# Performance work log

Measured on AMD Instinct MI355X. Metric: run time of the kernel, lower is better.

## Reference

```python
import jax, jax.numpy as jnp
import numpy as np

N = 8192
FEAT = 128
HID = 128
EMB = 128
NHEADS = 2
RO_HID = 256
G_EMB = 128
ALPHA = 0.2          # LeakyReLU negative slope
NEG_INF = -9e15      # matches -9000000000000000.0 in the torch source


def _xavier(k, shape, gain=1.0):
    fan_in, fan_out = shape[-2], shape[-1]
    s = gain * np.sqrt(2.0 / (fan_in + fan_out))
    return jax.random.normal(k, shape, jnp.float32) * jnp.float32(s)


def setup_inputs() -> dict:
    key = jax.random.key(0)
    ks = jax.random.split(key, 10)
    adj = jax.random.randint(ks[0], (N, N), 0, 2, jnp.int32)          # dense 0/1 adjacency
    x = jax.random.normal(ks[1], (N, FEAT), jnp.float32)
    W_heads = _xavier(ks[2], (NHEADS, FEAT, HID), gain=1.414)
    a_heads = _xavier(ks[3], (NHEADS, 2 * HID, 1), gain=1.414)
    W_out = _xavier(ks[4], (NHEADS * HID, EMB), gain=1.414)
    a_out = _xavier(ks[5], (2 * EMB, 1), gain=1.414)
    ge_w1 = _xavier(ks[6], (FEAT + EMB, RO_HID))
    ge_b1 = jnp.zeros((RO_HID,), jnp.float32)
    ge_w2 = _xavier(ks[7], (RO_HID, G_EMB))
    ge_b2 = jnp.zeros((G_EMB,), jnp.float32)
    return dict(adj=adj, feature_matrix=x, W_heads=W_heads, a_heads=a_heads,
                W_out=W_out, a_out=a_out, ge_w1=ge_w1, ge_b1=ge_b1,
                ge_w2=ge_w2, ge_b2=ge_b2, supply=0)


def _gat_layer(x, mask, W, a, concat):
    # Faithful to GraphAttentionLayer: e_ij = leakyrelu([Wh_i || Wh_j] @ a).
    # The concat-then-matmul decomposes exactly as Wh@a[:F] + (Wh@a[F:])^T,
    # avoiding the O(N^2 * 2F) a_input tensor while computing identical math.
    Wh = x @ W                                   # [N, F]
    F_out = W.shape[1]
    f1 = (Wh @ a[:F_out]).squeeze(-1)            # [N]
    f2 = (Wh @ a[F_out:]).squeeze(-1)            # [N]
    e = jax.nn.leaky_relu(f1[:, None] + f2[None, :], ALPHA)   # [N, N]
    e = jnp.where(mask, e, jnp.float32(NEG_INF))
    att = jax.nn.softmax(e, axis=1)              # dropout is identity in eval mode
    h = att @ Wh                                 # [N, F]
    return jax.nn.elu(h) if concat else h


def reference(adj, feature_matrix, W_heads, a_heads, W_out, a_out,
              ge_w1, ge_b1, ge_w2, ge_b2, supply):
    mask = adj > 0
    # GAT: multi-head layer 1 (concat), then out_att (no concat) + elu
    heads = [_gat_layer(feature_matrix, mask, W_heads[i], a_heads[i], True)
             for i in range(NHEADS)]
    h = jnp.concatenate(heads, axis=1)           # [N, NHEADS*HID]
    node_emb = jax.nn.elu(_gat_layer(h, mask, W_out, a_out, False))  # [N, EMB]
    # GraphEmb readout (mode='mean')
    combined = jnp.concatenate([feature_matrix, node_emb], axis=1)   # [N, FEAT+EMB]
    h1 = jax.nn.relu(combined @ ge_w1 + ge_b1)
    h2 = jax.nn.relu(h1 @ ge_w2 + ge_b2)
    graph_emb = jnp.mean(h2, axis=0)             # [G_EMB]
    return node_emb, graph_emb
```

## Files before the change

### kernel.cpp

```cpp
#include <hip/hip_runtime.h>
#include <hip/hip_bf16.h>

typedef unsigned short u16;
typedef __attribute__((ext_vector_type(4))) float f32x4;
typedef __attribute__((ext_vector_type(8))) short bf16x8;
typedef __attribute__((ext_vector_type(4))) unsigned short u16x4;

#define N 8192
#define LOG2E 1.4426950408889634f

__device__ __forceinline__ float bf2f(u16 u){
  union { float f; unsigned int i; } v; v.i = ((unsigned int)u) << 16; return v.f;
}
__device__ __forceinline__ u16 f2bf(float f){
  union { float f; unsigned int i; } v; v.f = f;
  unsigned int r = v.i + 0x7fffu + ((v.i >> 16) & 1u);
  return (u16)(r >> 16);
}
__device__ __forceinline__ f32x4 mfma16(bf16x8 a, bf16x8 b, f32x4 c){
  return __builtin_amdgcn_mfma_f32_16x16x32_bf16(a, b, c, 0, 0, 0);
}
__device__ __forceinline__ unsigned int fkey_enc(float f){
  unsigned int u = __float_as_uint(f);
  return (u & 0x80000000u) ? ~u : (u | 0x80000000u);
}
__device__ __forceinline__ float fkey_dec(unsigned int k){
  unsigned int u = (k & 0x80000000u) ? (k ^ 0x80000000u) : ~k;
  return __uint_as_float(u);
}
__device__ __forceinline__ void gload16(const void* g, void* l){
  __builtin_amdgcn_global_load_lds(
      (const __attribute__((address_space(1))) unsigned int*)(g),
      (__attribute__((address_space(3))) unsigned int*)(l), 16, 0, 0);
}

__global__ __launch_bounds__(256) void k_pack(const int* __restrict__ adj,
                                              unsigned long long* __restrict__ packed){
  const int wid = blockIdx.x * 4 + (threadIdx.x >> 6);
  const int lane = threadIdx.x & 63;
  const size_t base = (size_t)wid * 128;
  #pragma unroll 4
  for (int g = 0; g < 128; ++g){
    const size_t grp = base + g;
    const int v = adj[grp * 64 + lane];
    const unsigned long long m = __ballot(v != 0);
    if (lane == 0){
      const unsigned int lo = (unsigned int)m, hi = (unsigned int)(m >> 32);
      const unsigned int olo = __builtin_amdgcn_perm(hi, lo, 0x05010400u);
      const unsigned int ohi = __builtin_amdgcn_perm(hi, lo, 0x07030602u);
      packed[grp] = ((unsigned long long)ohi << 32) | olo;
    }
  }
}

__global__ __launch_bounds__(256) void k_prep(
    const float* __restrict__ x, const float* __restrict__ Wh, const float* __restrict__ Wo,
    const float* __restrict__ g1, const float* __restrict__ g2,
    const float* __restrict__ ah, const float* __restrict__ ao,
    u16* __restrict__ xbf, u16* __restrict__ comb,
    u16* __restrict__ wth, u16* __restrict__ wot,
    u16* __restrict__ g1t, u16* __restrict__ g2t,
    float* __restrict__ wa, unsigned int* __restrict__ fkey, float* __restrict__ csum)
{
  const int b = blockIdx.x, t = threadIdx.x;
  if (b < 1024){
    const int idx = b * 256 + t;
    f32x4 v = ((const f32x4*)x)[idx];
    u16x4 h;
    #pragma unroll
    for (int e = 0; e < 4; ++e) h[e] = f2bf(v[e]);
    ((u16x4*)xbf)[idx] = h;
    const int i = idx >> 5, c4 = (idx & 31) * 4;
    *(u16x4*)(comb + (size_t)i * 256 + c4) = h;
  } else if (b < 1152){
    const int rel = (b - 1024) * 256 + t;
    const int head = rel >> 14, win = rel & 16383;
    const int n = win >> 7, k = win & 127;
    wth[rel] = f2bf(Wh[(head << 14) + k * 128 + n]);
  } else if (b < 1280){
    const int rel = (b - 1152) * 256 + t;
    const int n = rel >> 8, k = rel & 255;
    wot[rel] = f2bf(Wo[k * 128 + n]);
  } else if (b < 1536){
    const int rel = (b - 1280) * 256 + t;
    const int n = rel >> 8, k = rel & 255;
    g1t[rel] = f2bf(g1[k * 256 + n]);
  } else if (b < 1664){
    const int rel = (b - 1536) * 256 + t;
    const int n = rel >> 8, k = rel & 255;
    g2t[rel] = f2bf(g2[k * 128 + n]);
  } else if (b < 1667){
    const int z = b - 1664;
    if (z < 2){
      if (t < 128){
        float a1 = 0.f, a2 = 0.f;
        for (int c = 0; c < 128; ++c){
          const float w = Wh[(size_t)z * 16384 + t * 128 + c];
          a1 += w * ah[z * 256 + c];
          a2 += w * ah[z * 256 + 128 + c];
        }
        wa[z * 128 + t] = a1; wa[256 + z * 128 + t] = a2;
      }
    } else {
      if (t < 256){
        float a1 = 0.f, a2 = 0.f;
        for (int c = 0; c < 128; ++c){
          const float w = Wo[(size_t)t * 128 + c];
          a1 += w * ao[c];
          a2 += w * ao[128 + c];
        }
        wa[512 + t] = a1; wa[768 + t] = a2;
      }
    }
  } else {
    if (t < 128) csum[t] = 0.f;
    if (t < 4) fkey[t] = 0u;
  }
}

__global__ __launch_bounds__(256) void k_gemv1(const float* __restrict__ x, const float* __restrict__ wa,
                                               float* __restrict__ f1s, float* __restrict__ f2s,
                                               unsigned int* __restrict__ fkey){
  const int h = blockIdx.y;
  const float* wa1 = wa + h * 128;
  const float* wa2 = wa + 256 + h * 128;
  const int lane = threadIdx.x & 63, w = threadIdx.x >> 6;
  const int r16 = lane & 15, g4 = lane >> 4;
  const int row = blockIdx.x * 16 + w * 4 + g4;
  const float* xr = x + (size_t)row * 128 + r16 * 8;
  f32x4 x0 = *(const f32x4*)(xr);
  f32x4 x1 = *(const f32x4*)(xr + 4);
  f32x4 wA0 = *(const f32x4*)(wa1 + r16 * 8);
  f32x4 wA1 = *(const f32x4*)(wa1 + r16 * 8 + 4);
  f32x4 wB0 = *(const f32x4*)(wa2 + r16 * 8);
  f32x4 wB1 = *(const f32x4*)(wa2 + r16 * 8 + 4);
  float d1 = 0.f, d2 = 0.f;
  #pragma unroll
  for (int e = 0; e < 4; ++e){
    d1 += x0[e] * wA0[e] + x1[e] * wA1[e];
    d2 += x0[e] * wB0[e] + x1[e] * wB1[e];
  }
  d1 += __shfl_xor(d1, 1); d1 += __shfl_xor(d1, 2); d1 += __shfl_xor(d1, 4); d1 += __shfl_xor(d1, 8);
  d2 += __shfl_xor(d2, 1); d2 += __shfl_xor(d2, 2); d2 += __shfl_xor(d2, 4); d2 += __shfl_xor(d2, 8);
  const float d1s = d1 * LOG2E, d2s = d2 * LOG2E;
  if (r16 == 0){
    f1s[(size_t)h * N + row] = d1s;
    f2s[(size_t)h * N + row] = d2s;
  }
  float m = d2s;
  m = fmaxf(m, __shfl_xor(m, 16)); m = fmaxf(m, __shfl_xor(m, 32));
  if (lane == 0) atomicMax(fkey + h, fkey_enc(m));
}

__global__ __launch_bounds__(256) void k_gemv2(const u16* __restrict__ hbf,
                                               const float* __restrict__ wao1, const float* __restrict__ wao2,
                                               float* __restrict__ f1s, float* __restrict__ f2s,
                                               unsigned int* __restrict__ fkey){
  const int lane = threadIdx.x & 63, w = threadIdx.x >> 6;
  const int r16 = lane & 15, g4 = lane >> 4;
  const int row = blockIdx.x * 16 + w * 4 + g4;
  bf16x8 h0 = *(const bf16x8*)(hbf + (size_t)row * 256 + r16 * 16);
  bf16x8 h1 = *(const bf16x8*)(hbf + (size_t)row * 256 + r16 * 16 + 8);
  float d1 = 0.f, d2 = 0.f;
  #pragma unroll
  for (int e = 0; e < 8; ++e){
    const float v0 = bf2f((u16)h0[e]), v1 = bf2f((u16)h1[e]);
    d1 += v0 * wao1[r16 * 16 + e] + v1 * wao1[r16 * 16 + 8 + e];
    d2 += v0 * wao2[r16 * 16 + e] + v1 * wao2[r16 * 16 + 8 + e];
  }
  d1 += __shfl_xor(d1, 1); d1 += __shfl_xor(d1, 2); d1 += __shfl_xor(d1, 4); d1 += __shfl_xor(d1, 8);
  d2 += __shfl_xor(d2, 1); d2 += __shfl_xor(d2, 2); d2 += __shfl_xor(d2, 4); d2 += __shfl_xor(d2, 8);
  const float d1s = d1 * LOG2E, d2s = d2 * LOG2E;
  if (r16 == 0){
    f1s[row] = d1s;
    f2s[row] = d2s;
  }
  float m = d2s;
  m = fmaxf(m, __shfl_xor(m, 16)); m = fmaxf(m, __shfl_xor(m, 32));
  if (lane == 0) atomicMax(fkey, fkey_enc(m));
}

__global__ __launch_bounds__(256) void k_gemm_at(const u16* __restrict__ A_all, const u16* __restrict__ B,
                                                 u16* __restrict__ outT_all, int K){
  const int head = blockIdx.y;
  const u16* A = A_all + (size_t)head * 128 * K;
  u16* outT = outT_all + (size_t)head * 1048576;
  const int lane = threadIdx.x & 63, w = threadIdx.x >> 6;
  const int r16 = lane & 15, g4 = lane >> 4;
  const size_t ib = (size_t)blockIdx.x * 64 + w * 16;
  f32x4 acc[8];
  #pragma unroll
  for (int cg = 0; cg < 8; ++cg) acc[cg] = (f32x4){0,0,0,0};
  for (int kk = 0; kk < K; kk += 32){
    bf16x8 b = *(const bf16x8*)(B + (ib + r16) * (size_t)K + kk + g4 * 8);
    #pragma unroll
    for (int cg = 0; cg < 8; ++cg){
      bf16x8 a = *(const bf16x8*)(A + (size_t)(cg * 16 + r16) * K + kk + g4 * 8);
      acc[cg] = mfma16(a, b, acc[cg]);
    }
  }
  const int jp = w * 16 + r16;
  u16* tb = outT + (size_t)blockIdx.x * 8192;
  #pragma unroll
  for (int cg = 0; cg < 8; ++cg)
    #pragma unroll
    for (int q = 0; q < 4; ++q){
      const int c = cg * 16 + g4 * 4 + q;
      tb[c * 64 + (jp ^ ((c & 7) << 3))] = f2bf(acc[cg][q]);
    }
}

template<int S>
__global__ __launch_bounds__(256, 2) void k_attn(
    const unsigned char* __restrict__ pk,
    const u16* __restrict__ whT_all,
    const float* __restrict__ f1_all, const float* __restrict__ f2_all,
    const unsigned int* __restrict__ fkey,
    u16* __restrict__ part, float* __restrict__ pl)
{
  __shared__ __align__(16) u16 tile[2][8192];
  const int h = blockIdx.z;
  const int s = blockIdx.y;
  const float* f2 = f2_all + (size_t)h * N;
  const float fmax = fkey_dec(fkey[h]);
  const int w = threadIdx.x >> 6;
  const int lane = threadIdx.x & 63;
  const int r16 = lane & 15, g4 = lane >> 4;
  const size_t ibase = (size_t)blockIdx.x * 128 + w * 32;
  constexpr int TPS = 128 / S;
  const int t0 = s * TPS, t1 = t0 + TPS;
  const char* gt = (const char*)whT_all + (size_t)h * 2097152;

  float c1[2], c2[2], lsum[2];
  f32x4 acc[2][8];
  #pragma unroll
  for (int rg = 0; rg < 2; ++rg){
    const float f1v = f1_all[(size_t)h * N + ibase + rg * 16 + r16];
    const float y = f1v + fmax;
    const float mrow = fmaxf(y, 0.2f * y);
    c1[rg] = f1v - mrow;
    c2[rg] = fmaf(0.2f, f1v, -mrow);
    lsum[rg] = 0.f;
    #pragma unroll
    for (int ct = 0; ct < 8; ++ct) acc[rg][ct] = (f32x4){0,0,0,0};
  }

  const int swz = (r16 & 7) << 3;
  const int off0 = r16 * 64 + ((g4 * 8) ^ swz);
  const unsigned char* pkr0 = pk + (ibase + r16) * 1024 + g4 * 2;
  const unsigned char* pkr1 = pkr0 + 16 * 1024;

  auto stage = [&](int buf, int tt){
    const char* src = gt + (size_t)tt * 16384 + w * 4096 + lane * 16;
    char* dst = ((char*)&tile[0][0]) + buf * 16384 + w * 4096;
    #pragma unroll
    for (int k = 0; k < 4; ++k)
      gload16(src + k * 1024, dst + k * 1024);
  };

  stage(0, t0);
  for (int t = t0; t < t1; ++t){
    const int cur = (t - t0) & 1;
    __syncthreads();
    if (t + 1 < t1) stage(cur ^ 1, t + 1);
    const unsigned int bits0 = *(const unsigned short*)(pkr0 + t * 8);
    const unsigned int bits1 = *(const unsigned short*)(pkr1 + t * 8);
    const u16* lp = &tile[cur][0];
    #pragma unroll
    for (int k2 = 0; k2 < 2; ++k2){
      const float* fjp = f2 + t * 64 + k2 * 32 + g4 * 8;
      f32x4 fa = *(const f32x4*)(fjp);
      f32x4 fb = *(const f32x4*)(fjp + 4);
      bf16x8 pa0, pa1;
      {
        const unsigned int bb = (bits0 >> (k2 * 8)) & 0xFFu;
        union { __hip_bfloat162 h2[4]; bf16x8 v8; } u;
        #pragma unroll
        for (int xp = 0; xp < 4; ++xp){
          const float s0 = (xp < 2) ? fa[2 * xp] : fb[2 * xp - 4];
          const float s1 = (xp < 2) ? fa[2 * xp + 1] : fb[2 * xp - 3];
          float p0 = __builtin_amdgcn_exp2f(fmaxf(s0 + c1[0], fmaf(s0, 0.2f, c2[0])));
          float p1 = __builtin_amdgcn_exp2f(fmaxf(s1 + c1[0], fmaf(s1, 0.2f, c2[0])));
          p0 = ((bb >> (2 * xp)) & 1u) ? p0 : 0.f;
          p1 = ((bb >> (2 * xp + 1)) & 1u) ? p1 : 0.f;
          lsum[0] += p0 + p1;
          u.h2[xp] = __float22bfloat162_rn(make_float2(p0, p1));
        }
        pa0 = u.v8;
      }
      {
        const unsigned int bb = (bits1 >> (k2 * 8)) & 0xFFu;
        union { __hip_bfloat162 h2[4]; bf16x8 v8; } u;
        #pragma unroll
        for (int xp = 0; xp < 4; ++xp){
          const float s0 = (xp < 2) ? fa[2 * xp] : fb[2 * xp - 4];
          const float s1 = (xp < 2) ? fa[2 * xp + 1] : fb[2 * xp - 3];
          float p0 = __builtin_amdgcn_exp2f(fmaxf(s0 + c1[1], fmaf(s0, 0.2f, c2[1])));
          float p1 = __builtin_amdgcn_exp2f(fmaxf(s1 + c1[1], fmaf(s1, 0.2f, c2[1])));
          p0 = ((bb >> (2 * xp)) & 1u) ? p0 : 0.f;
          p1 = ((bb >> (2 * xp + 1)) & 1u) ? p1 : 0.f;
          lsum[1] += p0 + p1;
          u.h2[xp] = __float22bfloat162_rn(make_float2(p0, p1));
        }
        pa1 = u.v8;
      }
      const int offk = off0 ^ (k2 << 5);
      #pragma unroll
      for (int ct = 0; ct < 8; ++ct){
        bf16x8 b = *(const bf16x8*)(lp + offk + ct * 1024);
        acc[0][ct] = mfma16(pa0, b, acc[0][ct]);
        acc[1][ct] = mfma16(pa1, b, acc[1][ct]);
      }
    }
  }

  const int plane = h * S + s;
  #pragma unroll
  for (int rg = 0; rg < 2; ++rg){
    const int tile_row = (int)(ibase >> 4) + rg;
    u16* pp = part + ((size_t)plane * 512 + tile_row) * 2048;
    #pragma unroll
    for (int ct = 0; ct < 8; ++ct)
      #pragma unroll
      for (int q = 0; q < 4; ++q)
        pp[(ct * 4 + q) * 64 + lane] = f2bf(acc[rg][ct][q]);
    float lv = lsum[rg];
    lv += __shfl_xor(lv, 16); lv += __shfl_xor(lv, 32);
    if (lane < 16) pl[(size_t)plane * N + ibase + rg * 16 + lane] = lv;
  }
}

template<int S, bool L2>
__global__ __launch_bounds__(256) void k_attn_merge(
    const u16* __restrict__ part, const float* __restrict__ pl,
    u16* __restrict__ hbf, float* __restrict__ nodeout, u16* __restrict__ comb)
{
  const int h = blockIdx.y;
  const int idx = blockIdx.x * 256 + threadIdx.x;
  const int i = idx >> 5, c4 = (idx & 31) * 4;
  const int tl = i >> 4, r = i & 15;
  const size_t off = (size_t)tl * 2048 + (size_t)(((c4 >> 4) * 4 + (r & 3)) * 64 + ((r >> 2) & 3) * 16 + (c4 & 15));
  f32x4 a = (f32x4){0,0,0,0};
  float L = 0.f;
  #pragma unroll
  for (int s = 0; s < S; ++s){
    const size_t plane = h * S + s;
    u16x4 v = *(const u16x4*)(part + plane * (size_t)(N * 128) + off);
    a[0] += bf2f(v[0]); a[1] += bf2f(v[1]); a[2] += bf2f(v[2]); a[3] += bf2f(v[3]);
    L += pl[plane * (size_t)N + i];
  }
  const float linv = 1.f / L;
  u16x4 hv;
  #pragma unroll
  for (int e = 0; e < 4; ++e){
    float o = a[e] * linv;
    o = (o > 0.f) ? o : (__expf(o) - 1.f);
    a[e] = o;
    hv[e] = f2bf(o);
  }
  if constexpr (!L2){
    *(u16x4*)(hbf + (size_t)i * 256 + h * 128 + c4) = hv;
  } else {
    *(f32x4*)(nodeout + (size_t)i * 128 + c4) = a;
    *(u16x4*)(comb + (size_t)i * 256 + 128 + c4) = hv;
  }
}

template<bool STORE, bool COLSUM>
__global__ __launch_bounds__(256) void k_gemm_row(
    const u16* __restrict__ A, const u16* __restrict__ BT,
    const float* __restrict__ bias,
    u16* __restrict__ out, float* __restrict__ csum,
    int K, int Ntot)
{
  const int lane = threadIdx.x & 63, w = threadIdx.x >> 6;
  const int r16 = lane & 15, g4 = lane >> 4;
  const size_t rbase = (size_t)blockIdx.x * 64 + w * 16;
  const int cbase = blockIdx.y * 128;
  f32x4 acc[8];
  #pragma unroll
  for (int ct = 0; ct < 8; ++ct) acc[ct] = (f32x4){0,0,0,0};
  for (int kk = 0; kk < K; kk += 32){
    bf16x8 af = *(const bf16x8*)(A + (rbase + r16) * (size_t)K + kk + g4 * 8);
    #pragma unroll
    for (int ct = 0; ct < 8; ++ct){
      bf16x8 bfr = *(const bf16x8*)(BT + (size_t)(cbase + ct * 16 + r16) * K + kk + g4 * 8);
      acc[ct] = mfma16(af, bfr, acc[ct]);
    }
  }
  #pragma unroll
  for (int ct = 0; ct < 8; ++ct){
    const float bv = bias[cbase + ct * 16 + r16];
    float sacc = 0.f;
    #pragma unroll
    for (int q = 0; q < 4; ++q){
      float v = acc[ct][q] + bv;
      v = fmaxf(v, 0.f);
      if constexpr (STORE)
        out[(rbase + g4 * 4 + q) * (size_t)Ntot + cbase + ct * 16 + r16] = f2bf(v);
      sacc += v;
    }
    if constexpr (COLSUM){
      sacc += __shfl_xor(sacc, 16); sacc += __shfl_xor(sacc, 32);
      if (lane < 16) atomicAdd(&csum[cbase + ct * 16 + lane], sacc);
    }
  }
}

__global__ void k_final(const float* __restrict__ csum, float* __restrict__ out){
  out[threadIdx.x] = csum[threadIdx.x] * (1.f / 8192.f);
}

extern "C" void kernel_launch(void* const* d_in, const int* in_sizes, int n_in,
                              void* d_out, int out_size, void* d_ws, size_t ws_size,
                              hipStream_t stream) {
  const int*   adj = (const int*)d_in[0];
  const float* x   = (const float*)d_in[1];
  const float* Wh  = (const float*)d_in[2];
  const float* ah  = (const float*)d_in[3];
  const float* Wo  = (const float*)d_in[4];
  const float* ao  = (const float*)d_in[5];
  const float* g1  = (const float*)d_in[6];
  const float* b1  = (const float*)d_in[7];
  const float* g2  = (const float*)d_in[8];
  const float* b2  = (const float*)d_in[9];
  float* outp = (float*)d_out;
  char* ws = (char*)d_ws;

  constexpr size_t PK   = 0;
  constexpr size_t PART = 8388608;
  constexpr size_t PL   = 25165824;
  constexpr size_t XBF  = 25427968;
  constexpr size_t WHT1 = 27525120;
  constexpr size_t WHT2 = 31719424;
  constexpr size_t HBF  = 33816576;
  constexpr size_t COMB = 38010880;
  constexpr size_t H1RO = WHT1;
  constexpr size_t F1S  = 42205184;
  constexpr size_t F2S  = 42270720;
  constexpr size_t CSUM = 42336256;
  constexpr size_t WTH  = 42336768;
  constexpr size_t WOT  = 42402304;
  constexpr size_t G1T  = 42467840;
  constexpr size_t G2T  = 42598912;
  constexpr size_t WA   = 42664448;
  constexpr size_t FKEY = 42668544;

  k_pack<<<2048, 256, 0, stream>>>(adj, (unsigned long long*)(ws + PK));
  k_prep<<<1668, 256, 0, stream>>>(x, Wh, Wo, g1, g2, ah, ao,
      (u16*)(ws + XBF), (u16*)(ws + COMB), (u16*)(ws + WTH), (u16*)(ws + WOT),
      (u16*)(ws + G1T), (u16*)(ws + G2T),
      (float*)(ws + WA), (unsigned int*)(ws + FKEY), (float*)(ws + CSUM));

  k_gemv1<<<dim3(512, 2), 256, 0, stream>>>(x, (const float*)(ws + WA),
      (float*)(ws + F1S), (float*)(ws + F2S), (unsigned int*)(ws + FKEY));
  k_gemm_at<<<dim3(128, 2), 256, 0, stream>>>((const u16*)(ws + WTH), (const u16*)(ws + XBF),
                                              (u16*)(ws + WHT1), 128);
  k_attn<4><<<dim3(64, 4, 2), 256, 0, stream>>>(
      (const unsigned char*)(ws + PK), (const u16*)(ws + WHT1),
      (const float*)(ws + F1S), (const float*)(ws + F2S), (const unsigned int*)(ws + FKEY),
      (u16*)(ws + PART), (float*)(ws + PL));
  k_attn_merge<4, false><<<dim3(1024, 2), 256, 0, stream>>>(
      (const u16*)(ws + PART), (const float*)(ws + PL),
      (u16*)(ws + HBF), nullptr, nullptr);

  k_gemv2<<<dim3(512, 1), 256, 0, stream>>>((const u16*)(ws + HBF),
      (const float*)(ws + WA) + 512, (const float*)(ws + WA) + 768,
      (float*)(ws + F1S), (float*)(ws + F2S), (unsigned int*)(ws + FKEY) + 2);
  k_gemm_at<<<dim3(128, 1), 256, 0, stream>>>((const u16*)(ws + WOT), (const u16*)(ws + HBF),
                                              (u16*)(ws + WHT2), 256);
  k_attn<8><<<dim3(64, 8, 1), 256, 0, stream>>>(
      (const unsigned char*)(ws + PK), (const u16*)(ws + WHT2),
      (const float*)(ws + F1S), (const float*)(ws + F2S), (const unsigned int*)(ws + FKEY) + 2,
      (u16*)(ws + PART), (float*)(ws + PL));
  k_attn_merge<8, true><<<dim3(1024, 1), 256, 0, stream>>>(
      (const u16*)(ws + PART), (const float*)(ws + PL),
      nullptr, outp, (u16*)(ws + COMB));

  k_gemm_row<true, false><<<dim3(128, 2), 256, 0, stream>>>(
      (const u16*)(ws + COMB), (const u16*)(ws + G1T), b1,
      (u16*)(ws + H1RO), nullptr, 256, 256);
  k_gemm_row<false, true><<<dim3(128, 1), 256, 0, stream>>>(
      (const u16*)(ws + H1RO), (const u16*)(ws + G2T), b2,
      nullptr, (float*)(ws + CSUM), 256, 128);
  k_final<<<1, 128, 0, stream>>>((const float*)(ws + CSUM), outp + (size_t)N * 128);
}
```

Before: 703.2 us.

## Vectorize adjacency packing, prefetch mask bits and B fragments, raise attention occupancy and splits

Rewrites the adjacency packing kernel to have each wave read whole rows with 16-byte loads. It builds bytes from ballots directly in the layout the attention kernel consumes. The attention kernel now prefetches the next tile's mask bits and hoists LDS B-fragment loads ahead of the exp computation, with launch bounds raised to 4 blocks per CU. The key-dimension split count doubles for both layers, which grows the partial buffer and shifts workspace offsets. The extra splits add merge traffic, and the higher occupancy target may force register spills.

```diff
diff --git a/kernel.cpp b/kernel.cpp
--- a/kernel.cpp
+++ b/kernel.cpp
@@ -5,6 +5,7 @@
 typedef __attribute__((ext_vector_type(4))) float f32x4;
 typedef __attribute__((ext_vector_type(8))) short bf16x8;
 typedef __attribute__((ext_vector_type(4))) unsigned short u16x4;
+typedef __attribute__((ext_vector_type(4))) int i32x4;
 
 #define N 8192
 #define LOG2E 1.4426950408889634f
@@ -35,20 +36,41 @@
 }
 
 __global__ __launch_bounds__(256) void k_pack(const int* __restrict__ adj,
-                                              unsigned long long* __restrict__ packed){
+                                              unsigned char* __restrict__ pk){
   const int wid = blockIdx.x * 4 + (threadIdx.x >> 6);
   const int lane = threadIdx.x & 63;
-  const size_t base = (size_t)wid * 128;
-  #pragma unroll 4
-  for (int g = 0; g < 128; ++g){
-    const size_t grp = base + g;
-    const int v = adj[grp * 64 + lane];
-    const unsigned long long m = __ballot(v != 0);
-    if (lane == 0){
-      const unsigned int lo = (unsigned int)m, hi = (unsigned int)(m >> 32);
-      const unsigned int olo = __builtin_amdgcn_perm(hi, lo, 0x05010400u);
-      const unsigned int ohi = __builtin_amdgcn_perm(hi, lo, 0x07030602u);
-      packed[grp] = ((unsigned long long)ohi << 32) | olo;
+  const int half = lane >> 5, b = lane & 31;
+  const int sh0 = (b >> 3) * 16 + (b & 7) * 2;
+  const int outoff = half * 32 + ((b >> 3) << 3) + (((b & 3) << 1) | ((b >> 2) & 1));
+  for (int r = 0; r < 4; ++r){
+    const size_t row = (size_t)wid * 4 + r;
+    const int* ar = adj + row * 8192;
+    unsigned char* pr = pk + row * 1024;
+    for (int it = 0; it < 16; ++it){
+      i32x4 v0 = *(const i32x4*)(ar + it * 512 + lane * 4);
+      i32x4 v1 = *(const i32x4*)(ar + it * 512 + 256 + lane * 4);
+      unsigned long long A0 = __ballot(v0[0] != 0);
+      unsigned long long A1 = __ballot(v0[1] != 0);
+      unsigned long long A2 = __ballot(v0[2] != 0);
+      unsigned long long A3 = __ballot(v0[3] != 0);
+      unsigned long long C0 = __ballot(v1[0] != 0);
+      unsigned long long C1 = __ballot(v1[1] != 0);
+      unsigned long long C2 = __ballot(v1[2] != 0);
+      unsigned long long C3 = __ballot(v1[3] != 0);
+      const unsigned long long B0 = half ? C0 : A0;
+      const unsigned long long B1 = half ? C1 : A1;
+      const unsigned long long B2 = half ? C2 : A2;
+      const unsigned long long B3 = half ? C3 : A3;
+      unsigned int byte =
+          (unsigned int)((B0 >> sh0) & 1ull)
+        | ((unsigned int)((B1 >> sh0) & 1ull) << 1)
+        | ((unsigned int)((B2 >> sh0) & 1ull) << 2)
+        | ((unsigned int)((B3 >> sh0) & 1ull) << 3)
+        | ((unsigned int)((B0 >> (sh0 + 1)) & 1ull) << 4)
+        | ((unsigned int)((B1 >> (sh0 + 1)) & 1ull) << 5)
+        | ((unsigned int)((B2 >> (sh0 + 1)) & 1ull) << 6)
+        | ((unsigned int)((B3 >> (sh0 + 1)) & 1ull) << 7);
+      pr[it * 64 + outoff] = (unsigned char)byte;
     }
   }
 }
@@ -211,7 +233,7 @@
 }
 
 template<int S>
-__global__ __launch_bounds__(256, 2) void k_attn(
+__global__ __launch_bounds__(256, 4) void k_attn(
     const unsigned char* __restrict__ pk,
     const u16* __restrict__ whT_all,
     const float* __restrict__ f1_all, const float* __restrict__ f2_all,
@@ -259,15 +281,25 @@
   };
 
   stage(0, t0);
+  unsigned int bits0 = *(const unsigned short*)(pkr0 + t0 * 8);
+  unsigned int bits1 = *(const unsigned short*)(pkr1 + t0 * 8);
+
   for (int t = t0; t < t1; ++t){
     const int cur = (t - t0) & 1;
     __syncthreads();
     if (t + 1 < t1) stage(cur ^ 1, t + 1);
-    const unsigned int bits0 = *(const unsigned short*)(pkr0 + t * 8);
-    const unsigned int bits1 = *(const unsigned short*)(pkr1 + t * 8);
+    unsigned int nb0 = bits0, nb1 = bits1;
+    if (t + 1 < t1){
+      nb0 = *(const unsigned short*)(pkr0 + (t + 1) * 8);
+      nb1 = *(const unsigned short*)(pkr1 + (t + 1) * 8);
+    }
     const u16* lp = &tile[cur][0];
     #pragma unroll
     for (int k2 = 0; k2 < 2; ++k2){
+      const int offk = off0 ^ (k2 << 5);
+      bf16x8 bfr[8];
+      #pragma unroll
+      for (int ct = 0; ct < 8; ++ct) bfr[ct] = *(const bf16x8*)(lp + offk + ct * 1024);
       const float* fjp = f2 + t * 64 + k2 * 32 + g4 * 8;
       f32x4 fa = *(const f32x4*)(fjp);
       f32x4 fb = *(const f32x4*)(fjp + 4);
@@ -304,14 +336,13 @@
         }
         pa1 = u.v8;
       }
-      const int offk = off0 ^ (k2 << 5);
       #pragma unroll
       for (int ct = 0; ct < 8; ++ct){
-        bf16x8 b = *(const bf16x8*)(lp + offk + ct * 1024);
-        acc[0][ct] = mfma16(pa0, b, acc[0][ct]);
-        acc[1][ct] = mfma16(pa1, b, acc[1][ct]);
+        acc[0][ct] = mfma16(pa0, bfr[ct], acc[0][ct]);
+        acc[1][ct] = mfma16(pa1, bfr[ct], acc[1][ct]);
       }
     }
+    bits0 = nb0; bits1 = nb1;
   }
 
   const int plane = h * S + s;
@@ -429,24 +460,24 @@
 
   constexpr size_t PK   = 0;
   constexpr size_t PART = 8388608;
-  constexpr size_t PL   = 25165824;
-  constexpr size_t XBF  = 25427968;
-  constexpr size_t WHT1 = 27525120;
-  constexpr size_t WHT2 = 31719424;
-  constexpr size_t HBF  = 33816576;
-  constexpr size_t COMB = 38010880;
+  constexpr size_t PL   = 41943040;
+  constexpr size_t XBF  = 42467328;
+  constexpr size_t WHT1 = 44564480;
+  constexpr size_t WHT2 = 48758784;
+  constexpr size_t HBF  = 50855936;
+  constexpr size_t COMB = 55050240;
   constexpr size_t H1RO = WHT1;
-  constexpr size_t F1S  = 42205184;
-  constexpr size_t F2S  = 42270720;
-  constexpr size_t CSUM = 42336256;
-  constexpr size_t WTH  = 42336768;
-  constexpr size_t WOT  = 42402304;
-  constexpr size_t G1T  = 42467840;
-  constexpr size_t G2T  = 42598912;
-  constexpr size_t WA   = 42664448;
-  constexpr size_t FKEY = 42668544;
-
-  k_pack<<<2048, 256, 0, stream>>>(adj, (unsigned long long*)(ws + PK));
+  constexpr size_t F1S  = 59244544;
+  constexpr size_t F2S  = 59310080;
+  constexpr size_t CSUM = 59375616;
+  constexpr size_t WTH  = 59376128;
+  constexpr size_t WOT  = 59441664;
+  constexpr size_t G1T  = 59507200;
+  constexpr size_t G2T  = 59638272;
+  constexpr size_t WA   = 59703808;
+  constexpr size_t FKEY = 59707904;
+
+  k_pack<<<512, 256, 0, stream>>>(adj, (unsigned char*)(ws + PK));
   k_prep<<<1668, 256, 0, stream>>>(x, Wh, Wo, g1, g2, ah, ao,
       (u16*)(ws + XBF), (u16*)(ws + COMB), (u16*)(ws + WTH), (u16*)(ws + WOT),
       (u16*)(ws + G1T), (u16*)(ws + G2T),
@@ -456,11 +487,11 @@
       (float*)(ws + F1S), (float*)(ws + F2S), (unsigned int*)(ws + FKEY));
   k_gemm_at<<<dim3(128, 2), 256, 0, stream>>>((const u16*)(ws + WTH), (const u16*)(ws + XBF),
                                               (u16*)(ws + WHT1), 128);
-  k_attn<4><<<dim3(64, 4, 2), 256, 0, stream>>>(
+  k_attn<8><<<dim3(64, 8, 2), 256, 0, stream>>>(
       (const unsigned char*)(ws + PK), (const u16*)(ws + WHT1),
       (const float*)(ws + F1S), (const float*)(ws + F2S), (const unsigned int*)(ws + FKEY),
       (u16*)(ws + PART), (float*)(ws + PL));
-  k_attn_merge<4, false><<<dim3(1024, 2), 256, 0, stream>>>(
+  k_attn_merge<8, false><<<dim3(1024, 2), 256, 0, stream>>>(
       (const u16*)(ws + PART), (const float*)(ws + PL),
       (u16*)(ws + HBF), nullptr, nullptr);
 
@@ -469,11 +500,11 @@
       (float*)(ws + F1S), (float*)(ws + F2S), (unsigned int*)(ws + FKEY) + 2);
   k_gemm_at<<<dim3(128, 1), 256, 0, stream>>>((const u16*)(ws + WOT), (const u16*)(ws + HBF),
                                               (u16*)(ws + WHT2), 256);
-  k_attn<8><<<dim3(64, 8, 1), 256, 0, stream>>>(
+  k_attn<16><<<dim3(64, 16, 1), 256, 0, stream>>>(
       (const unsigned char*)(ws + PK), (const u16*)(ws + WHT2),
       (const float*)(ws + F1S), (const float*)(ws + F2S), (const unsigned int*)(ws + FKEY) + 2,
       (u16*)(ws + PART), (float*)(ws + PL));
-  k_attn_merge<8, true><<<dim3(1024, 1), 256, 0, stream>>>(
+  k_attn_merge<16, true><<<dim3(1024, 1), 256, 0, stream>>>(
       (const u16*)(ws + PART), (const float*)(ws + PL),
       nullptr, outp, (u16*)(ws + COMB));
 
```

Result: faster. 668.1 us (-5.0%).
